# Kernel tuning notes

Hardware: AMD Instinct MI355X
Metric: run time of the kernel (lower is better)

The kernel has to match this reference:

```python
import jax, jax.numpy as jnp
import numpy as np

H = 12           # num_heads
D_MODEL = 768
SCALE = (D_MODEL // H) ** -0.5  # qk_scale default: head_dim**-0.5


def _attn_mask(q, k, v, mask):
    # sim: (b, i, j); mask broadcast over query dim (mask.unsqueeze(1) in torch)
    sim = jnp.einsum('bid,bjd->bij', q, k) + mask[:, None, :]
    a = jax.nn.softmax(sim, axis=-1)
    return jnp.einsum('bij,bjd->bid', a, v)


def setup_inputs() -> dict:
    key = jax.random.key(0)
    k0, k1, k2, k3 = jax.random.split(key, 4)
    B, F, n, D = 16, 8, 196, 768
    N = 1 + F * n  # cls + frames*patches = 1569
    x = jax.random.normal(k0, (B, N, D), jnp.float32)
    x_mask = jax.random.normal(k1, (B, N), jnp.float32)  # additive attention mask
    Wqkv = jax.random.normal(k2, (3 * D, D), jnp.float32) * (D ** -0.5)
    Wproj = jax.random.normal(k3, (D, D), jnp.float32) * (D ** -0.5)
    bproj = jnp.zeros((D,), jnp.float32)
    return {"x": x, "x_mask": x_mask, "Wqkv": Wqkv, "Wproj": Wproj,
            "bproj": bproj, "f": F}


def reference(x, x_mask, Wqkv, Wproj, bproj, f):
    B, N, D = x.shape
    h = H
    d = D // h
    # qkv projection (qkv_bias=False), split into q,k,v
    qkv = x @ Wqkv.T                       # (B, N, 3D)
    q, k, v = jnp.split(qkv, 3, axis=-1)

    def to_heads(t):  # 'b n (h d) -> (b h) n d'
        return t.reshape(B, N, h, d).transpose(0, 2, 1, 3).reshape(B * h, N, d)

    q, k, v = map(to_heads, (q, k, v))
    mask = jnp.repeat(x_mask, h, axis=0)   # repeat_interleave over heads: (B*h, N)

    q = q * SCALE
    cls_q, q_ = q[:, :1], q[:, 1:]
    cls_k, k_ = k[:, :1], k[:, 1:]
    cls_v, v_ = v[:, :1], v[:, 1:]
    cls_mask, mask_ = mask[:, :1], mask[:, 1:]

    # cls token attends to everything
    cls_out = _attn_mask(cls_q, k, v, mask)            # (B*h, 1, d)

    # spatial attention: 'b (f n) d -> (b f) n d'
    n = (N - 1) // f
    q_ = q_.reshape(B * h * f, n, d)
    k_ = k_.reshape(B * h * f, n, d)
    v_ = v_.reshape(B * h * f, n, d)
    mask_ = mask_.reshape(B * h * f, n)

    # prepend cls k/v/mask to every frame group (r = f)
    cls_k = jnp.repeat(cls_k, f, axis=0)               # (B*h*f, 1, d)
    cls_v = jnp.repeat(cls_v, f, axis=0)
    cls_m = jnp.repeat(cls_mask, f, axis=0)            # (B*h*f, 1)
    k_ = jnp.concatenate([cls_k, k_], axis=1)          # (B*h*f, n+1, d)
    v_ = jnp.concatenate([cls_v, v_], axis=1)
    m2 = jnp.concatenate([cls_m, mask_], axis=1)       # (B*h*f, n+1)

    out = _attn_mask(q_, k_, v_, m2)                   # (B*h*f, n, d)
    out = out.reshape(B * h, f * n, d)                 # '(b f) n d -> b (f n) d'
    out = jnp.concatenate([cls_out, out], axis=1)      # (B*h, N, d)
    out = out.reshape(B, h, N, d).transpose(0, 2, 1, 3).reshape(B, N, D)
    return out @ Wproj.T + bproj
```

## Files before the change

### kernel.cpp

```cpp
#include <hip/hip_runtime.h>
#include <hip/hip_bf16.h>
#include <stdint.h>

#define Hh 12
#define Dm 768
#define Bb 16
#define Nt 1569
#define Ff 8
#define NC 196
#define BH 192
#define Mr 25104
#define CPW 224
#define VTW (8*CPW)
#define PLD 232
#define CLD 132

typedef __attribute__((ext_vector_type(8))) short bf16x8;
typedef __attribute__((ext_vector_type(4))) float f32x4;

typedef const __attribute__((address_space(1))) uint32_t guint;
typedef __attribute__((address_space(3))) uint32_t luint;

static __device__ __forceinline__ float bf2f(unsigned short u) {
  union { unsigned int i; float f; } v; v.i = ((unsigned int)u) << 16; return v.f;
}
static __device__ __forceinline__ unsigned short f2bf(float f) {
  __hip_bfloat16 h = __float2bfloat16(f);
  return __builtin_bit_cast(unsigned short, h);
}

__global__ void cast3_k(const float4* __restrict__ s0, ushort4* __restrict__ d0, int n0,
                        const float4* __restrict__ s1, ushort4* __restrict__ d1, int n1,
                        const float4* __restrict__ s2, ushort4* __restrict__ d2, int n2) {
  int nTot = n0 + n1 + n2;
  for (int i = blockIdx.x * blockDim.x + threadIdx.x; i < nTot; i += gridDim.x * blockDim.x) {
    const float4* s; ushort4* d; int off;
    if (i < n0) { s = s0; d = d0; off = i; }
    else if (i < n0 + n1) { s = s1; d = d1; off = i - n0; }
    else { s = s2; d = d2; off = i - n0 - n1; }
    float4 f = s[off];
    ushort4 u;
    u.x = f2bf(f.x); u.y = f2bf(f.y); u.z = f2bf(f.z); u.w = f2bf(f.w);
    d[off] = u;
  }
}

template<int MODE>
__global__ __launch_bounds__(256) void gemm_k(
    const __hip_bfloat16* __restrict__ A,
    const __hip_bfloat16* __restrict__ W,
    int M, int K,
    __hip_bfloat16* __restrict__ qh, __hip_bfloat16* __restrict__ kh,
    __hip_bfloat16* __restrict__ vT, __hip_bfloat16* __restrict__ vcls,
    const float* __restrict__ bias, float* __restrict__ outp)
{
  __shared__ __align__(16) unsigned short shmem[24576];

  const int tid = threadIdx.x;
  const int lane = tid & 63, wid = tid >> 6;
  const int waveM = wid >> 1, waveN = wid & 1;

  const int gridN = gridDim.x;
  const int nwg = gridDim.x * gridDim.y;
  int bid = blockIdx.y * gridN + blockIdx.x;
  int q8 = nwg >> 3, r8 = nwg & 7;
  int xcd = bid & 7, lid = bid >> 3;
  int swz = (xcd < r8 ? xcd * (q8 + 1) : r8 * (q8 + 1) + (xcd - r8) * q8) + lid;
  const int mBase = (swz / gridN) * 128, nBase = (swz % gridN) * 128;

  const int l15 = lane & 15, lg = lane >> 4;

  int arow0, brow0, ks0, arow1, brow1, ks1;
  {
    int seg = tid;
    int row = seg >> 2; ks0 = seg & 3;
    arow0 = mBase + row; if (arow0 >= M) arow0 = M - 1;
    brow0 = nBase + row;
    seg = 256 + tid;
    row = seg >> 2; ks1 = seg & 3;
    arow1 = mBase + row; if (arow1 >= M) arow1 = M - 1;
    brow1 = nBase + row;
  }
  auto STAGE = [&](int buf, int kt) {
    unsigned short* base = shmem + buf * 8192;
    __builtin_amdgcn_global_load_lds((guint*)(A + (size_t)arow0 * K + kt * 32 + ks0 * 8),
                                     (luint*)&base[tid * 8], 16, 0, 0);
    __builtin_amdgcn_global_load_lds((guint*)(W + (size_t)brow0 * K + kt * 32 + ks0 * 8),
                                     (luint*)&base[4096 + tid * 8], 16, 0, 0);
    __builtin_amdgcn_global_load_lds((guint*)(A + (size_t)arow1 * K + kt * 32 + ks1 * 8),
                                     (luint*)&base[(256 + tid) * 8], 16, 0, 0);
    __builtin_amdgcn_global_load_lds((guint*)(W + (size_t)brow1 * K + kt * 32 + ks1 * 8),
                                     (luint*)&base[4096 + (256 + tid) * 8], 16, 0, 0);
  };

  f32x4 acc[4][4] = {};
  const int nkt = K >> 5;

  STAGE(0, 0);
  STAGE(1, 1);
  asm volatile("s_waitcnt vmcnt(4)" ::: "memory");
  __builtin_amdgcn_s_barrier();
  __builtin_amdgcn_sched_barrier(0);

  int cur = 0;
  for (int kt = 0; kt < nkt; ++kt) {
    if (kt + 2 < nkt) {
      int b2 = cur + 2; if (b2 >= 3) b2 -= 3;
      STAGE(b2, kt + 2);
    }
    const unsigned short* base = shmem + cur * 8192;
    bf16x8 aF[4], bF[4];
#pragma unroll
    for (int i = 0; i < 4; ++i) {
      aF[i] = *reinterpret_cast<const bf16x8*>(&base[(waveM * 64 + i * 16 + l15) * 32 + lg * 8]);
      bF[i] = *reinterpret_cast<const bf16x8*>(&base[4096 + (waveN * 64 + i * 16 + l15) * 32 + lg * 8]);
    }
#pragma unroll
    for (int mi = 0; mi < 4; ++mi)
#pragma unroll
      for (int ni = 0; ni < 4; ++ni)
        acc[mi][ni] = __builtin_amdgcn_mfma_f32_16x16x32_bf16(aF[mi], bF[ni], acc[mi][ni], 0, 0, 0);
    __builtin_amdgcn_sched_barrier(0);
    if (kt + 2 < nkt) {
      asm volatile("s_waitcnt vmcnt(4)" ::: "memory");
    } else {
      asm volatile("s_waitcnt vmcnt(0)" ::: "memory");
    }
    __builtin_amdgcn_s_barrier();
    __builtin_amdgcn_sched_barrier(0);
    cur = cur + 1; if (cur >= 3) cur -= 3;
  }

  if (MODE == 1) {
    const bool fullM = (mBase + 128 <= M);
#pragma unroll
    for (int mi = 0; mi < 4; ++mi)
#pragma unroll
      for (int ni = 0; ni < 4; ++ni)
#pragma unroll
        for (int r = 0; r < 4; ++r) {
          int grow = mBase + waveM * 64 + mi * 16 + lg * 4 + r;
          if (!fullM && grow >= M) continue;
          int gcol = nBase + waveN * 64 + ni * 16 + l15;
          outp[(size_t)grow * Dm + gcol] = acc[mi][ni][r] + bias[gcol];
        }
    return;
  }

  const int which = nBase / Dm;
  const int headBase = (nBase - which * Dm) >> 6;
  const float scl = (which == 0) ? 0.125f : 1.f;
  const bool fullM = (mBase + 128 <= M);

  if (fullM) {
    if (which < 2) {
#pragma unroll
      for (int mi = 0; mi < 4; ++mi)
#pragma unroll
        for (int ni = 0; ni < 4; ++ni)
#pragma unroll
          for (int r = 0; r < 4; ++r)
            shmem[(waveM * 64 + mi * 16 + lg * 4 + r) * CLD + (waveN * 64 + ni * 16 + l15)]
                = f2bf(acc[mi][ni][r] * scl);
      __syncthreads();
      __hip_bfloat16* dst = (which == 0) ? qh : kh;
      int row = tid >> 1, h = tid & 1;
      int grow = mBase + row;
      int b = grow / Nt, i = grow - b * Nt;
      const uint2* sp = reinterpret_cast<const uint2*>(&shmem[row * CLD + h * 64]);
      uint2* dp = reinterpret_cast<uint2*>(
          dst + ((size_t)(b * Hh + headBase + h) * Nt + i) * 64);
#pragma unroll
      for (int j = 0; j < 16; ++j) dp[j] = sp[j];
    } else {
#pragma unroll
      for (int mi = 0; mi < 4; ++mi)
#pragma unroll
        for (int ni = 0; ni < 4; ++ni)
#pragma unroll
          for (int r = 0; r < 4; ++r)
            shmem[(waveN * 64 + ni * 16 + l15) * CLD + (waveM * 64 + mi * 16 + lg * 4 + r)]
                = f2bf(acc[mi][ni][r]);
      __syncthreads();
      int lc = tid & 127, rhalf = tid >> 7;
      int h = lc >> 6, dc = lc & 63;
      int head = headBase + h;
#pragma unroll
      for (int g = 0; g < 8; ++g) {
        int row0 = rhalf * 64 + g * 8;
        int grow0 = mBase + row0;
        int b = grow0 / Nt, i0 = grow0 - b * Nt;
        const unsigned short* sp = &shmem[lc * CLD + row0];
        if (i0 >= 1 && i0 + 8 <= Nt) {
          int j0 = i0 - 1, cc = j0 / NC, key = j0 - cc * NC;
          if (key + 8 <= NC) {
            int bh = b * Hh + head;
            __hip_bfloat16* p = vT + ((size_t)bh * 64 + dc) * VTW + cc * CPW + key;
            if ((key & 1) == 0) {
              const unsigned int* s4 = reinterpret_cast<const unsigned int*>(sp);
              unsigned int* d4 = reinterpret_cast<unsigned int*>(p);
              d4[0] = s4[0]; d4[1] = s4[1]; d4[2] = s4[2]; d4[3] = s4[3];
            } else {
#pragma unroll
              for (int j = 0; j < 8; ++j)
                p[j] = __builtin_bit_cast(__hip_bfloat16, sp[j]);
            }
            continue;
          }
        }
#pragma unroll
        for (int j = 0; j < 8; ++j) {
          int grow = grow0 + j;
          int bb = grow / Nt, ii = grow - bb * Nt;
          int bh2 = bb * Hh + head;
          unsigned short val = sp[j];
          if (ii == 0) {
            vcls[bh2 * 64 + dc] = __builtin_bit_cast(__hip_bfloat16, val);
          } else {
            int jj = ii - 1, cc2 = jj / NC, k2 = jj - cc2 * NC;
            vT[((size_t)bh2 * 64 + dc) * VTW + cc2 * CPW + k2]
                = __builtin_bit_cast(__hip_bfloat16, val);
          }
        }
      }
    }
  } else {
#pragma unroll
    for (int mi = 0; mi < 4; ++mi)
#pragma unroll
      for (int ni = 0; ni < 4; ++ni)
#pragma unroll
        for (int r = 0; r < 4; ++r) {
          int grow = mBase + waveM * 64 + mi * 16 + lg * 4 + r;
          if (grow >= M) continue;
          int gcol = nBase + waveN * 64 + ni * 16 + l15;
          float v = acc[mi][ni][r];
          int b = grow / Nt, i = grow - b * Nt;
          int hcol = gcol - which * Dm;
          int head = hcol >> 6, dc = hcol & 63;
          int bh = b * Hh + head;
          if (which == 0) {
            qh[((size_t)bh * Nt + i) * 64 + dc] = __float2bfloat16(v * 0.125f);
          } else if (which == 1) {
            kh[((size_t)bh * Nt + i) * 64 + dc] = __float2bfloat16(v);
          } else {
            if (i == 0) vcls[bh * 64 + dc] = __float2bfloat16(v);
            else {
              int j = i - 1; int cc = j / NC, key = j - cc * NC;
              vT[((size_t)bh * 64 + dc) * VTW + cc * CPW + key] = __float2bfloat16(v);
            }
          }
        }
  }
}

__global__ __launch_bounds__(256, 1) void attn_k(
    const __hip_bfloat16* __restrict__ qh, const __hip_bfloat16* __restrict__ kh,
    const __hip_bfloat16* __restrict__ vT, const __hip_bfloat16* __restrict__ vcls,
    const float* __restrict__ x_mask, __hip_bfloat16* __restrict__ ao)
{
  __shared__ __align__(16) __hip_bfloat16 ldsK[208 * 64];
  __shared__ __align__(16) __hip_bfloat16 ldsV[64 * 256];
  __shared__ __align__(16) __hip_bfloat16 ldsP[4][16 * PLD];
  __shared__ float sS[Nt];
  __shared__ float qv[64];
  __shared__ float red[256];

  const int bidx = blockIdx.x;
  const int tid = threadIdx.x;

  if (bidx < BH) {
    const int bh = bidx, b = bh / Hh, head = bh - b * Hh;
    if (tid < 64) qv[tid] = __bfloat162float(qh[((size_t)bh * Nt) * 64 + tid]);
    __syncthreads();
    float lmax = -1e30f;
    for (int j = tid; j < Nt; j += 256) {
      const __hip_bfloat16* kr = kh + ((size_t)bh * Nt + j) * 64;
      float dot = 0.f;
#pragma unroll
      for (int d0 = 0; d0 < 64; d0 += 8) {
        bf16x8 kv = *reinterpret_cast<const bf16x8*>(kr + d0);
#pragma unroll
        for (int i = 0; i < 8; ++i) dot += qv[d0 + i] * bf2f((unsigned short)kv[i]);
      }
      float s = dot + x_mask[b * Nt + j];
      sS[j] = s;
      lmax = fmaxf(lmax, s);
    }
    red[tid] = lmax; __syncthreads();
    for (int off = 128; off > 0; off >>= 1) {
      if (tid < off) red[tid] = fmaxf(red[tid], red[tid + off]);
      __syncthreads();
    }
    float m = red[0]; __syncthreads();
    float lsum = 0.f;
    for (int j = tid; j < Nt; j += 256) { float e = __expf(sS[j] - m); sS[j] = e; lsum += e; }
    red[tid] = lsum; __syncthreads();
    for (int off = 128; off > 0; off >>= 1) {
      if (tid < off) red[tid] += red[tid + off];
      __syncthreads();
    }
    float rden = 1.f / red[0]; __syncthreads();
    int dc = tid & 63, part = tid >> 6;
    float partial = 0.f;
    if (part == 0) partial = sS[0] * __bfloat162float(vcls[bh * 64 + dc]);
    const __hip_bfloat16* vrow = vT + ((size_t)bh * 64 + dc) * VTW;
    for (int cc = part * 2; cc < part * 2 + 2; ++cc) {
      int base = 1 + cc * NC;
      const __hip_bfloat16* vc2 = vrow + cc * CPW;
      int key = 0;
      for (; key + 8 <= NC; key += 8) {
        bf16x8 vv = *reinterpret_cast<const bf16x8*>(vc2 + key);
#pragma unroll
        for (int i = 0; i < 8; ++i)
          partial += sS[base + key + i] * bf2f((unsigned short)vv[i]);
      }
      for (; key < NC; ++key)
        partial += sS[base + key] * __bfloat162float(vc2[key]);
    }
    red[tid] = partial; __syncthreads();
    if (tid < 64) {
      float o = (red[tid] + red[tid + 64] + red[tid + 128] + red[tid + 192]) * rden;
      ao[((size_t)b * Nt) * Dm + head * 64 + dc] = __float2bfloat16(o);
    }
    return;
  }

  const int g = bidx - BH;
  const int bh = g >> 3, c = g & 7;
  const int b = bh / Hh, head = bh - b * Hh;
  const int lane = tid & 63, wid = tid >> 6;
  const int l15 = lane & 15, lg = lane >> 4;

  const int kbase = 1 + c * NC;

#pragma unroll
  for (int it = 0; it < 7; ++it) {
    int idx = it * 256 + tid;
    if (idx < 1664) {
      int row = idx >> 3, c16 = idx & 7;
      int token = kbase + row; if (token > Nt - 1) token = Nt - 1;
      __builtin_amdgcn_global_load_lds(
          (guint*)(kh + ((size_t)bh * Nt + token) * 64 + ((c16 ^ (row & 7)) * 8)),
          (luint*)&ldsK[idx * 8], 16, 0, 0);
    }
  }
#pragma unroll
  for (int it = 0; it < 7; ++it) {
    int idx = it * 256 + tid;
    int dc = idx / 28, u = idx - dc * 28;
    uint4 v = *reinterpret_cast<const uint4*>(
        vT + ((size_t)bh * 64 + dc) * VTW + c * CPW + u * 8);
    *reinterpret_cast<uint4*>(&ldsV[dc * 256 + ((u ^ (dc & 7)) * 8)]) = v;
  }
  __syncthreads();

  __hip_bfloat16* myP = ldsP[wid];

  const __hip_bfloat16* kc = kh + (size_t)bh * Nt * 64;
  bf16x8 ck0 = *reinterpret_cast<const bf16x8*>(kc + lg * 8);
  bf16x8 ck1 = *reinterpret_cast<const bf16x8*>(kc + 32 + lg * 8);
  const float maskCls = x_mask[b * Nt];

  for (int rt = wid; rt < 13; rt += 4) {
    int qlrow = rt * 16 + l15;
    int qtok = 1 + c * NC + qlrow; if (qtok > Nt - 1) qtok = Nt - 1;
    const __hip_bfloat16* qp = qh + ((size_t)bh * Nt + qtok) * 64;
    bf16x8 aQ0 = *reinterpret_cast<const bf16x8*>(qp + lg * 8);
    bf16x8 aQ1 = *reinterpret_cast<const bf16x8*>(qp + 32 + lg * 8);

    float pc0 = 0.f;
#pragma unroll
    for (int i = 0; i < 8; ++i)
      pc0 += bf2f((unsigned short)aQ0[i]) * bf2f((unsigned short)ck0[i])
           + bf2f((unsigned short)aQ1[i]) * bf2f((unsigned short)ck1[i]);
    pc0 += __shfl_xor(pc0, 16);
    pc0 += __shfl_xor(pc0, 32);
    pc0 += maskCls;

    f32x4 S[13];
    float mv[13];
#define LD_MM(i) { \
    int row = (i) * 16 + l15; \
    bf16x8 kb0 = *reinterpret_cast<const bf16x8*>(&ldsK[row * 64 + ((lg ^ (l15 & 7)) * 8)]); \
    bf16x8 kb1 = *reinterpret_cast<const bf16x8*>(&ldsK[row * 64 + (((4 + lg) ^ (l15 & 7)) * 8)]); \
    mv[i] = (row < NC) ? x_mask[b * Nt + kbase + row] : -1e30f; \
    f32x4 sa = {}; \
    sa = __builtin_amdgcn_mfma_f32_16x16x32_bf16(aQ0, kb0, sa, 0, 0, 0); \
    sa = __builtin_amdgcn_mfma_f32_16x16x32_bf16(aQ1, kb1, sa, 0, 0, 0); \
    S[i][0] = sa[0] + mv[i]; S[i][1] = sa[1] + mv[i]; \
    S[i][2] = sa[2] + mv[i]; S[i][3] = sa[3] + mv[i]; }
    LD_MM(0) LD_MM(1) LD_MM(2) LD_MM(3) LD_MM(4) LD_MM(5) LD_MM(6)
    LD_MM(7) LD_MM(8) LD_MM(9) LD_MM(10) LD_MM(11) LD_MM(12)
#undef LD_MM

    float pcls[4], rden[4];
#pragma unroll
    for (int r = 0; r < 4; ++r) {
      float m = -1e30f;
#pragma unroll
      for (int nt = 0; nt < 13; ++nt) m = fmaxf(m, S[nt][r]);
      m = fmaxf(m, __shfl_xor(m, 1));
      m = fmaxf(m, __shfl_xor(m, 2));
      m = fmaxf(m, __shfl_xor(m, 4));
      m = fmaxf(m, __shfl_xor(m, 8));
      float sc = __shfl(pc0, lg * 4 + r);
      m = fmaxf(m, sc);
      float sum = 0.f;
#pragma unroll
      for (int nt = 0; nt < 13; ++nt) { float e = __expf(S[nt][r] - m); S[nt][r] = e; sum += e; }
      sum += __shfl_xor(sum, 1);
      sum += __shfl_xor(sum, 2);
      sum += __shfl_xor(sum, 4);
      sum += __shfl_xor(sum, 8);
      float pc = __expf(sc - m);
      pcls[r] = pc;
      rden[r] = 1.f / (sum + pc);
    }

#pragma unroll
    for (int nt = 0; nt < 13; ++nt)
#pragma unroll
      for (int r = 0; r < 4; ++r)
        myP[(lg * 4 + r) * PLD + nt * 16 + l15] = __float2bfloat16(S[nt][r]);
#pragma unroll
    for (int r = 0; r < 4; ++r)
      myP[l15 * PLD + 208 + lg * 4 + r] = __float2bfloat16(0.f);
    asm volatile("s_waitcnt lgkmcnt(0)" ::: "memory");
    __builtin_amdgcn_sched_barrier(0);

    f32x4 O[4] = {};
#define PVK(kt) { \
    bf16x8 aP = *reinterpret_cast<const bf16x8*>(&myP[l15 * PLD + (kt) * 32 + lg * 8]); \
    { int dc = 0 * 16 + l15; bf16x8 bV = *reinterpret_cast<const bf16x8*>(&ldsV[dc * 256 + ((((kt) * 4 + lg) ^ (l15 & 7)) * 8)]); \
      O[0] = __builtin_amdgcn_mfma_f32_16x16x32_bf16(aP, bV, O[0], 0, 0, 0); } \
    { int dc = 1 * 16 + l15; bf16x8 bV = *reinterpret_cast<const bf16x8*>(&ldsV[dc * 256 + ((((kt) * 4 + lg) ^ (l15 & 7)) * 8)]); \
      O[1] = __builtin_amdgcn_mfma_f32_16x16x32_bf16(aP, bV, O[1], 0, 0, 0); } \
    { int dc = 2 * 16 + l15; bf16x8 bV = *reinterpret_cast<const bf16x8*>(&ldsV[dc * 256 + ((((kt) * 4 + lg) ^ (l15 & 7)) * 8)]); \
      O[2] = __builtin_amdgcn_mfma_f32_16x16x32_bf16(aP, bV, O[2], 0, 0, 0); } \
    { int dc = 3 * 16 + l15; bf16x8 bV = *reinterpret_cast<const bf16x8*>(&ldsV[dc * 256 + ((((kt) * 4 + lg) ^ (l15 & 7)) * 8)]); \
      O[3] = __builtin_amdgcn_mfma_f32_16x16x32_bf16(aP, bV, O[3], 0, 0, 0); } }
    PVK(0) PVK(1) PVK(2) PVK(3) PVK(4) PVK(5) PVK(6)
#undef PVK

#pragma unroll
    for (int ni = 0; ni < 4; ++ni) {
      int dc = ni * 16 + l15;
      float vc = __bfloat162float(vcls[bh * 64 + dc]);
#pragma unroll
      for (int r = 0; r < 4; ++r) {
        int lrow = rt * 16 + lg * 4 + r;
        if (lrow < NC) {
          float o = (O[ni][r] + pcls[r] * vc) * rden[r];
          int tok = 1 + c * NC + lrow;
          ao[((size_t)b * Nt + tok) * Dm + head * 64 + dc] = __float2bfloat16(o);
        }
      }
    }
  }
}

extern "C" void kernel_launch(void* const* d_in, const int* in_sizes, int n_in,
                              void* d_out, int out_size, void* d_ws, size_t ws_size,
                              hipStream_t stream) {
  const float* x     = (const float*)d_in[0];
  const float* xmask = (const float*)d_in[1];
  const float* wqkv  = (const float*)d_in[2];
  const float* wproj = (const float*)d_in[3];
  const float* bproj = (const float*)d_in[4];
  float* outp = (float*)d_out;

  char* ws = (char*)d_ws;
  size_t off = 0;
  auto alloc = [&](size_t bytes) {
    char* p = ws + off;
    off += (bytes + 255) & ~(size_t)255;
    return p;
  };
  __hip_bfloat16* xb     = (__hip_bfloat16*)alloc((size_t)Mr * Dm * 2);
  __hip_bfloat16* wqkvb  = (__hip_bfloat16*)alloc((size_t)3 * Dm * Dm * 2);
  __hip_bfloat16* wprojb = (__hip_bfloat16*)alloc((size_t)Dm * Dm * 2);
  __hip_bfloat16* qh     = (__hip_bfloat16*)alloc((size_t)BH * Nt * 64 * 2);
  __hip_bfloat16* kh     = (__hip_bfloat16*)alloc((size_t)BH * Nt * 64 * 2);
  __hip_bfloat16* vT     = (__hip_bfloat16*)alloc((size_t)BH * 64 * VTW * 2);
  __hip_bfloat16* vcls   = (__hip_bfloat16*)alloc((size_t)BH * 64 * 2);
  __hip_bfloat16* ao = xb;

  cast3_k<<<2048, 256, 0, stream>>>((const float4*)x, (ushort4*)xb, Mr * Dm / 4,
                                    (const float4*)wqkv, (ushort4*)wqkvb, 3 * Dm * Dm / 4,
                                    (const float4*)wproj, (ushort4*)wprojb, Dm * Dm / 4);

  gemm_k<0><<<dim3(18, 197), 256, 0, stream>>>(xb, wqkvb, Mr, Dm, qh, kh, vT, vcls, nullptr, nullptr);

  attn_k<<<BH + BH * Ff, 256, 0, stream>>>(qh, kh, vT, vcls, xmask, ao);

  gemm_k<1><<<dim3(6, 197), 256, 0, stream>>>(ao, wprojb, Mr, Dm, nullptr, nullptr, nullptr, nullptr, bproj, outp);
}
```

Measured before the change: 337.0 us.

## Enlarge GEMM tiles to 256x256 with 8 waves, 4-stage pipeline and swizzled LDS

Both projection GEMMs move from 128x128 tiles with 4 waves to 256x256 tiles with 8 waves. Each wave now computes 128x64 in two MFMA halves, and global-to-LDS staging is split and interleaved between those halves. The pipeline grows to four LDS buffers, adds an XOR swizzle on the 16-byte column chunks to cut bank conflicts, and raises wave priority around the MFMA blocks. Larger tiles raise arithmetic intensity, but they cost far more LDS and registers and leave fewer workgroups, which worsens load balance and tail waste (M=25104 is not a multiple of 256).

```diff
diff --git a/kernel.cpp b/kernel.cpp
--- a/kernel.cpp
+++ b/kernel.cpp
@@ -13,7 +13,7 @@
 #define CPW 224
 #define VTW (8*CPW)
 #define PLD 232
-#define CLD 132
+#define CLD2 260
 
 typedef __attribute__((ext_vector_type(8))) short bf16x8;
 typedef __attribute__((ext_vector_type(4))) float f32x4;
@@ -46,7 +46,7 @@
 }
 
 template<int MODE>
-__global__ __launch_bounds__(256) void gemm_k(
+__global__ __launch_bounds__(512, 2) void gemm_k(
     const __hip_bfloat16* __restrict__ A,
     const __hip_bfloat16* __restrict__ W,
     int M, int K,
@@ -54,11 +54,12 @@
     __hip_bfloat16* __restrict__ vT, __hip_bfloat16* __restrict__ vcls,
     const float* __restrict__ bias, float* __restrict__ outp)
 {
-  __shared__ __align__(16) unsigned short shmem[24576];
+  __shared__ __align__(16) unsigned short shmem[66560];
 
   const int tid = threadIdx.x;
   const int lane = tid & 63, wid = tid >> 6;
-  const int waveM = wid >> 1, waveN = wid & 1;
+  const int wm = wid >> 2, wn = wid & 3;
+  const int l15 = lane & 15, lg = lane >> 4;
 
   const int gridN = gridDim.x;
   const int nwg = gridDim.x * gridDim.y;
@@ -66,82 +67,103 @@
   int q8 = nwg >> 3, r8 = nwg & 7;
   int xcd = bid & 7, lid = bid >> 3;
   int swz = (xcd < r8 ? xcd * (q8 + 1) : r8 * (q8 + 1) + (xcd - r8) * q8) + lid;
-  const int mBase = (swz / gridN) * 128, nBase = (swz % gridN) * 128;
-
-  const int l15 = lane & 15, lg = lane >> 4;
-
-  int arow0, brow0, ks0, arow1, brow1, ks1;
-  {
-    int seg = tid;
-    int row = seg >> 2; ks0 = seg & 3;
-    arow0 = mBase + row; if (arow0 >= M) arow0 = M - 1;
-    brow0 = nBase + row;
-    seg = 256 + tid;
-    row = seg >> 2; ks1 = seg & 3;
-    arow1 = mBase + row; if (arow1 >= M) arow1 = M - 1;
-    brow1 = nBase + row;
-  }
-  auto STAGE = [&](int buf, int kt) {
-    unsigned short* base = shmem + buf * 8192;
-    __builtin_amdgcn_global_load_lds((guint*)(A + (size_t)arow0 * K + kt * 32 + ks0 * 8),
-                                     (luint*)&base[tid * 8], 16, 0, 0);
-    __builtin_amdgcn_global_load_lds((guint*)(W + (size_t)brow0 * K + kt * 32 + ks0 * 8),
-                                     (luint*)&base[4096 + tid * 8], 16, 0, 0);
-    __builtin_amdgcn_global_load_lds((guint*)(A + (size_t)arow1 * K + kt * 32 + ks1 * 8),
-                                     (luint*)&base[(256 + tid) * 8], 16, 0, 0);
-    __builtin_amdgcn_global_load_lds((guint*)(W + (size_t)brow1 * K + kt * 32 + ks1 * 8),
-                                     (luint*)&base[4096 + (256 + tid) * 8], 16, 0, 0);
+  const int mBase = (swz / gridN) * 256, nBase = (swz % gridN) * 256;
+
+  auto STAGEA = [&](int bufi, int kt) {
+    unsigned short* dst = shmem + bufi * 16384;
+#pragma unroll
+    for (int h = 0; h < 2; ++h) {
+      int u = h * 512 + tid;
+      int row = u >> 2, c16 = u & 3;
+      int arow = mBase + row; if (arow >= M) arow = M - 1;
+      __builtin_amdgcn_global_load_lds(
+          (guint*)(A + (size_t)arow * K + kt * 32 + ((c16 ^ ((row >> 1) & 3)) * 8)),
+          (luint*)&dst[u * 8], 16, 0, 0);
+    }
   };
-
-  f32x4 acc[4][4] = {};
+  auto STAGEB = [&](int bufi, int kt) {
+    unsigned short* dst = shmem + bufi * 16384 + 8192;
+#pragma unroll
+    for (int h = 0; h < 2; ++h) {
+      int u = h * 512 + tid;
+      int row = u >> 2, c16 = u & 3;
+      int brow = nBase + row;
+      __builtin_amdgcn_global_load_lds(
+          (guint*)(W + (size_t)brow * K + kt * 32 + ((c16 ^ ((row >> 1) & 3)) * 8)),
+          (luint*)&dst[u * 8], 16, 0, 0);
+    }
+  };
+
+  f32x4 acc[8][4] = {};
   const int nkt = K >> 5;
-
-  STAGE(0, 0);
-  STAGE(1, 1);
-  asm volatile("s_waitcnt vmcnt(4)" ::: "memory");
+  const int rxor = (lg ^ ((l15 >> 1) & 3)) * 8;
+
+  STAGEA(0, 0); STAGEB(0, 0);
+  STAGEA(1, 1); STAGEB(1, 1);
+  STAGEA(2, 2); STAGEB(2, 2);
+  asm volatile("s_waitcnt vmcnt(8)" ::: "memory");
   __builtin_amdgcn_s_barrier();
   __builtin_amdgcn_sched_barrier(0);
 
-  int cur = 0;
+#pragma unroll 1
   for (int kt = 0; kt < nkt; ++kt) {
-    if (kt + 2 < nkt) {
-      int b2 = cur + 2; if (b2 >= 3) b2 -= 3;
-      STAGE(b2, kt + 2);
-    }
-    const unsigned short* base = shmem + cur * 8192;
+    const unsigned short* bufA = shmem + (kt & 3) * 16384;
+    const unsigned short* bufB = bufA + 8192;
+    const int b3 = (kt + 3) & 3;
     bf16x8 aF[4], bF[4];
 #pragma unroll
-    for (int i = 0; i < 4; ++i) {
-      aF[i] = *reinterpret_cast<const bf16x8*>(&base[(waveM * 64 + i * 16 + l15) * 32 + lg * 8]);
-      bF[i] = *reinterpret_cast<const bf16x8*>(&base[4096 + (waveN * 64 + i * 16 + l15) * 32 + lg * 8]);
-    }
+    for (int i = 0; i < 4; ++i)
+      aF[i] = *reinterpret_cast<const bf16x8*>(&bufA[(wm * 128 + i * 16 + l15) * 32 + rxor]);
+#pragma unroll
+    for (int i = 0; i < 4; ++i)
+      bF[i] = *reinterpret_cast<const bf16x8*>(&bufB[(wn * 64 + i * 16 + l15) * 32 + rxor]);
+    if (kt + 3 < nkt) STAGEA(b3, kt + 3);
+    asm volatile("s_waitcnt lgkmcnt(0)" ::: "memory");
+    __builtin_amdgcn_sched_barrier(0);
+    __builtin_amdgcn_s_setprio(1);
 #pragma unroll
     for (int mi = 0; mi < 4; ++mi)
 #pragma unroll
       for (int ni = 0; ni < 4; ++ni)
         acc[mi][ni] = __builtin_amdgcn_mfma_f32_16x16x32_bf16(aF[mi], bF[ni], acc[mi][ni], 0, 0, 0);
+    __builtin_amdgcn_s_setprio(0);
     __builtin_amdgcn_sched_barrier(0);
-    if (kt + 2 < nkt) {
-      asm volatile("s_waitcnt vmcnt(4)" ::: "memory");
+#pragma unroll
+    for (int i = 0; i < 4; ++i)
+      aF[i] = *reinterpret_cast<const bf16x8*>(&bufA[(wm * 128 + (4 + i) * 16 + l15) * 32 + rxor]);
+    if (kt + 3 < nkt) STAGEB(b3, kt + 3);
+    asm volatile("s_waitcnt lgkmcnt(0)" ::: "memory");
+    __builtin_amdgcn_sched_barrier(0);
+    __builtin_amdgcn_s_setprio(1);
+#pragma unroll
+    for (int mi = 0; mi < 4; ++mi)
+#pragma unroll
+      for (int ni = 0; ni < 4; ++ni)
+        acc[4 + mi][ni] = __builtin_amdgcn_mfma_f32_16x16x32_bf16(aF[mi], bF[ni], acc[4 + mi][ni], 0, 0, 0);
+    __builtin_amdgcn_s_setprio(0);
+    __builtin_amdgcn_sched_barrier(0);
+    if (kt + 1 < nkt) {
+      if (kt + 3 < nkt)      { asm volatile("s_waitcnt vmcnt(8)" ::: "memory"); }
+      else if (kt + 2 < nkt) { asm volatile("s_waitcnt vmcnt(4)" ::: "memory"); }
+      else                   { asm volatile("s_waitcnt vmcnt(0)" ::: "memory"); }
     } else {
       asm volatile("s_waitcnt vmcnt(0)" ::: "memory");
     }
     __builtin_amdgcn_s_barrier();
     __builtin_amdgcn_sched_barrier(0);
-    cur = cur + 1; if (cur >= 3) cur -= 3;
   }
 
   if (MODE == 1) {
-    const bool fullM = (mBase + 128 <= M);
-#pragma unroll
-    for (int mi = 0; mi < 4; ++mi)
+    const bool fullM = (mBase + 256 <= M);
+#pragma unroll
+    for (int mi = 0; mi < 8; ++mi)
 #pragma unroll
       for (int ni = 0; ni < 4; ++ni)
 #pragma unroll
         for (int r = 0; r < 4; ++r) {
-          int grow = mBase + waveM * 64 + mi * 16 + lg * 4 + r;
+          int grow = mBase + wm * 128 + mi * 16 + lg * 4 + r;
           if (!fullM && grow >= M) continue;
-          int gcol = nBase + waveN * 64 + ni * 16 + l15;
+          int gcol = nBase + wn * 64 + ni * 16 + l15;
           outp[(size_t)grow * Dm + gcol] = acc[mi][ni][r] + bias[gcol];
         }
     return;
@@ -150,47 +172,50 @@
   const int which = nBase / Dm;
   const int headBase = (nBase - which * Dm) >> 6;
   const float scl = (which == 0) ? 0.125f : 1.f;
-  const bool fullM = (mBase + 128 <= M);
+  const bool fullM = (mBase + 256 <= M);
 
   if (fullM) {
     if (which < 2) {
 #pragma unroll
-      for (int mi = 0; mi < 4; ++mi)
+      for (int mi = 0; mi < 8; ++mi)
 #pragma unroll
         for (int ni = 0; ni < 4; ++ni)
 #pragma unroll
           for (int r = 0; r < 4; ++r)
-            shmem[(waveM * 64 + mi * 16 + lg * 4 + r) * CLD + (waveN * 64 + ni * 16 + l15)]
+            shmem[(wm * 128 + mi * 16 + lg * 4 + r) * CLD2 + (wn * 64 + ni * 16 + l15)]
                 = f2bf(acc[mi][ni][r] * scl);
       __syncthreads();
       __hip_bfloat16* dst = (which == 0) ? qh : kh;
-      int row = tid >> 1, h = tid & 1;
+      int row = tid >> 1, hpart = tid & 1;
       int grow = mBase + row;
       int b = grow / Nt, i = grow - b * Nt;
-      const uint2* sp = reinterpret_cast<const uint2*>(&shmem[row * CLD + h * 64]);
-      uint2* dp = reinterpret_cast<uint2*>(
-          dst + ((size_t)(b * Hh + headBase + h) * Nt + i) * 64);
-#pragma unroll
-      for (int j = 0; j < 16; ++j) dp[j] = sp[j];
+#pragma unroll
+      for (int hh = 0; hh < 2; ++hh) {
+        int hsel = hpart * 2 + hh;
+        const uint2* sp = reinterpret_cast<const uint2*>(&shmem[row * CLD2 + hsel * 64]);
+        uint2* dp = reinterpret_cast<uint2*>(
+            dst + ((size_t)(b * Hh + headBase + hsel) * Nt + i) * 64);
+#pragma unroll
+        for (int j = 0; j < 16; ++j) dp[j] = sp[j];
+      }
     } else {
 #pragma unroll
-      for (int mi = 0; mi < 4; ++mi)
+      for (int mi = 0; mi < 8; ++mi)
 #pragma unroll
         for (int ni = 0; ni < 4; ++ni)
 #pragma unroll
           for (int r = 0; r < 4; ++r)
-            shmem[(waveN * 64 + ni * 16 + l15) * CLD + (waveM * 64 + mi * 16 + lg * 4 + r)]
+            shmem[(wn * 64 + ni * 16 + l15) * CLD2 + (wm * 128 + mi * 16 + lg * 4 + r)]
                 = f2bf(acc[mi][ni][r]);
       __syncthreads();
-      int lc = tid & 127, rhalf = tid >> 7;
-      int h = lc >> 6, dc = lc & 63;
-      int head = headBase + h;
-#pragma unroll
-      for (int g = 0; g < 8; ++g) {
-        int row0 = rhalf * 64 + g * 8;
+      int lc = tid & 255, rblk = tid >> 8;
+      int head = headBase + (lc >> 6), dc = lc & 63;
+#pragma unroll
+      for (int gi = 0; gi < 16; ++gi) {
+        int row0 = rblk * 128 + gi * 8;
         int grow0 = mBase + row0;
         int b = grow0 / Nt, i0 = grow0 - b * Nt;
-        const unsigned short* sp = &shmem[lc * CLD + row0];
+        const unsigned short* sp = &shmem[lc * CLD2 + row0];
         if (i0 >= 1 && i0 + 8 <= Nt) {
           int j0 = i0 - 1, cc = j0 / NC, key = j0 - cc * NC;
           if (key + 8 <= NC) {
@@ -226,14 +251,14 @@
     }
   } else {
 #pragma unroll
-    for (int mi = 0; mi < 4; ++mi)
+    for (int mi = 0; mi < 8; ++mi)
 #pragma unroll
       for (int ni = 0; ni < 4; ++ni)
 #pragma unroll
         for (int r = 0; r < 4; ++r) {
-          int grow = mBase + waveM * 64 + mi * 16 + lg * 4 + r;
+          int grow = mBase + wm * 128 + mi * 16 + lg * 4 + r;
           if (grow >= M) continue;
-          int gcol = nBase + waveN * 64 + ni * 16 + l15;
+          int gcol = nBase + wn * 64 + ni * 16 + l15;
           float v = acc[mi][ni][r];
           int b = grow / Nt, i = grow - b * Nt;
           int hcol = gcol - which * Dm;
@@ -490,9 +515,9 @@
                                     (const float4*)wqkv, (ushort4*)wqkvb, 3 * Dm * Dm / 4,
                                     (const float4*)wproj, (ushort4*)wprojb, Dm * Dm / 4);
 
-  gemm_k<0><<<dim3(18, 197), 256, 0, stream>>>(xb, wqkvb, Mr, Dm, qh, kh, vT, vcls, nullptr, nullptr);
+  gemm_k<0><<<dim3(9, 99), 512, 0, stream>>>(xb, wqkvb, Mr, Dm, qh, kh, vT, vcls, nullptr, nullptr);
 
   attn_k<<<BH + BH * Ff, 256, 0, stream>>>(qh, kh, vT, vcls, xmask, ao);
 
-  gemm_k<1><<<dim3(6, 197), 256, 0, stream>>>(ao, wprojb, Mr, Dm, nullptr, nullptr, nullptr, nullptr, bproj, outp);
+  gemm_k<1><<<dim3(3, 99), 512, 0, stream>>>(ao, wprojb, Mr, Dm, nullptr, nullptr, nullptr, nullptr, bproj, outp);
 }
```

New measurement: 362.1 us. 7.5% more time.
